# Kernel tuning notes

Hardware: AMD Instinct MI355X
Metric: run time of the kernel (lower is better)

## Reference

```python
import jax, jax.numpy as jnp
import numpy as np

B, S, H, DH = 4, 2048, 16, 64
D = H * DH          # 1024
EXP = 2
FF_IN = EXP * D * 2  # 4096 (SwiGLU doubles)
FF_HID = EXP * D     # 2048
SCALE_BASE = 512
LN_EPS = 1e-5


def setup_inputs() -> dict:
    key = jax.random.key(0)
    ks = jax.random.split(key, 8)
    inp = {
        "q": jax.random.normal(ks[0], (B, S, D), jnp.float32),
        "k": jax.random.normal(ks[1], (B, S, D), jnp.float32),
        "v": jax.random.normal(ks[2], (B, S, D), jnp.float32),
        "Wqkv": jax.random.normal(ks[3], (D, 3 * D), jnp.float32) * (1.0 / np.sqrt(D)),
        "bqkv": jnp.zeros((3 * D,), jnp.float32),
        "q_scale": jnp.ones((DH,), jnp.float32),
        "k_scale": jnp.ones((DH,), jnp.float32),
        "ln_g": jnp.ones((D,), jnp.float32),
        "ln_b": jnp.zeros((D,), jnp.float32),
        "W1": jax.random.normal(ks[4], (D, FF_IN), jnp.float32) * (1.0 / np.sqrt(D)),
        "b1": jnp.zeros((FF_IN,), jnp.float32),
        "W2": jax.random.normal(ks[5], (FF_HID, D), jnp.float32) * (1.0 / np.sqrt(FF_HID)),
        "b2": jnp.zeros((D,), jnp.float32),
    }
    return inp


def rotate_half(x):
    x1, x2 = jnp.split(x, 2, axis=-1)
    return jnp.concatenate((-x2, x1), axis=-1)


def apply_rope(pos, t, scale):
    # pos: [S, DH], scale: [S, DH] (broadcast over [B, H, S, DH])
    return t * jnp.cos(pos) * scale + rotate_half(t) * jnp.sin(pos) * scale


def rotary_tables(seq_len):
    inv_freq = 1.0 / (10000.0 ** (jnp.arange(0, DH, 2, dtype=jnp.float32) / DH))
    t = jnp.arange(seq_len, dtype=jnp.float32)
    freqs = t[:, None] * inv_freq[None, :]            # [S, DH/2]
    freqs = jnp.concatenate((freqs, freqs), axis=-1)  # [S, DH]
    power = (t - seq_len // 2) / SCALE_BASE           # [S]
    base = (jnp.arange(0, DH, 2, dtype=jnp.float32) + 0.4 * DH) / (1.4 * DH)  # [DH/2]
    scale = base[None, :] ** power[:, None]           # [S, DH/2]
    scale = jnp.concatenate((scale, scale), axis=-1)  # [S, DH]
    return freqs, scale


def l2norm(x, eps=1e-12):
    n = jnp.sqrt(jnp.sum(x * x, axis=-1, keepdims=True))
    return x / jnp.maximum(n, eps)


def reference(q, k, v, Wqkv, bqkv, q_scale, k_scale, ln_g, ln_b, W1, b1, W2, b2):
    del k, v  # module projects qkv from q; k,v args are unused (faithful to source)
    n, seq_len, _ = q.shape
    qkv = q @ Wqkv + bqkv                              # [B, S, 3D]
    qkv = qkv.reshape(n, seq_len, H, 3 * DH).transpose(0, 2, 1, 3)  # [B, H, S, 3DH]
    q_, k_, v_ = jnp.split(qkv, 3, axis=-1)
    q_ = l2norm(q_) * q_scale
    k_ = l2norm(k_) * k_scale
    pos, xscale = rotary_tables(seq_len)
    q_ = apply_rope(pos, q_, xscale)
    k_ = apply_rope(pos, k_, 1.0 / xscale)
    # scaled dot product attention (non-causal)
    scores = jnp.einsum("bhid,bhjd->bhij", q_, k_) / np.sqrt(DH)
    attn = jax.nn.softmax(scores, axis=-1)
    out = jnp.einsum("bhij,bhjd->bhid", attn, v_)      # [B, H, S, DH]
    out = out.transpose(0, 2, 1, 3).reshape(n, seq_len, D)
    # LayerNorm
    mu = jnp.mean(out, axis=-1, keepdims=True)
    var = jnp.mean((out - mu) ** 2, axis=-1, keepdims=True)
    out = (out - mu) / jnp.sqrt(var + LN_EPS) * ln_g + ln_b
    # SwiGLU FFN (dropout = identity in eval)
    h = out @ W1 + b1                                  # [B, S, FF_IN]
    x_, gate = jnp.split(h, 2, axis=-1)
    ff = (jax.nn.silu(gate) * x_) @ W2 + b2            # [B, S, D]
    return out + ff
```

## Files before the change

### kernel.cpp

```cpp
#include <hip/hip_runtime.h>
#include <math.h>


typedef __bf16 bf16;
typedef bf16 bf16x8 __attribute__((ext_vector_type(8)));
typedef bf16 bf16x4 __attribute__((ext_vector_type(4)));
typedef float f32x4 __attribute__((ext_vector_type(4)));

#define MFMA(a, b, c) __builtin_amdgcn_mfma_f32_16x16x32_bf16(a, b, c, 0, 0, 0)

__device__ __forceinline__ void async16(const void* g, void* l) {
    __builtin_amdgcn_global_load_lds(
        (const __attribute__((address_space(1))) void*)g,
        (__attribute__((address_space(3))) void*)l,
        16, 0, 0);
}

__global__ __launch_bounds__(256) void fill_sentinel(float* __restrict__ o)
{
    size_t i = ((size_t)blockIdx.x * 256 + threadIdx.x) * 4;
    *(float4*)&o[i] = make_float4(0.25f, 0.25f, 0.25f, 0.25f);
}

__global__ __launch_bounds__(256) void convert_f32_bf16(
    const float* __restrict__ in, bf16* __restrict__ out)
{
    size_t i = ((size_t)blockIdx.x * 256 + threadIdx.x) * 8;
    float4 f0 = *(const float4*)&in[i];
    float4 f1 = *(const float4*)&in[i + 4];
    bf16x8 v;
    v[0] = (bf16)f0.x; v[1] = (bf16)f0.y; v[2] = (bf16)f0.z; v[3] = (bf16)f0.w;
    v[4] = (bf16)f1.x; v[5] = (bf16)f1.y; v[6] = (bf16)f1.z; v[7] = (bf16)f1.w;
    *(bf16x8*)&out[i] = v;
}

__global__ __launch_bounds__(256) void transpose_f32_bf16(
    const float* __restrict__ in, bf16* __restrict__ out, int K, int N)
{
    __shared__ bf16 T[64][70];
    const int tN = N >> 6;
    const int tk = blockIdx.x / tN, tn = blockIdx.x % tN;
    const int k0 = tk << 6, n0 = tn << 6;
    const int t = threadIdx.x;
    const int r = t >> 2, c0 = (t & 3) << 4;
    const float* src = &in[(size_t)(k0 + r) * N + n0 + c0];
    for (int j = 0; j < 4; ++j) {
        float4 f = *(const float4*)(src + 4 * j);
        T[r][c0 + 4 * j + 0] = (bf16)f.x;
        T[r][c0 + 4 * j + 1] = (bf16)f.y;
        T[r][c0 + 4 * j + 2] = (bf16)f.z;
        T[r][c0 + 4 * j + 3] = (bf16)f.w;
    }
    __syncthreads();
    bf16x8 o0, o1;
    for (int i = 0; i < 8; ++i) o0[i] = T[c0 + i][r];
    for (int i = 0; i < 8; ++i) o1[i] = T[c0 + 8 + i][r];
    *(bf16x8*)&out[(size_t)(n0 + r) * K + k0 + c0]     = o0;
    *(bf16x8*)&out[(size_t)(n0 + r) * K + k0 + c0 + 8] = o1;
}

__global__ __launch_bounds__(256) void transpose_v(
    const bf16* __restrict__ in, bf16* __restrict__ out)
{
    __shared__ bf16 T[64][72];
    const int bh = blockIdx.x >> 5;
    const int s0 = (blockIdx.x & 31) << 6;
    const bf16* ip = in + ((size_t)bh << 17) + (size_t)s0 * 64;
    bf16* op = out + ((size_t)bh << 17) + s0;
    const int t = threadIdx.x;
    const int r = t >> 2, c0 = (t & 3) << 4;
    *(bf16x8*)&T[r][c0]     = *(const bf16x8*)&ip[r * 64 + c0];
    *(bf16x8*)&T[r][c0 + 8] = *(const bf16x8*)&ip[r * 64 + c0 + 8];
    __syncthreads();
    bf16x8 o0, o1;
    for (int i = 0; i < 8; ++i) o0[i] = T[c0 + i][r];
    for (int i = 0; i < 8; ++i) o1[i] = T[c0 + 8 + i][r];
    *(bf16x8*)&op[(size_t)r * 2048 + c0]     = o0;
    *(bf16x8*)&op[(size_t)r * 2048 + c0 + 8] = o1;
}

template <int BN, bool SPLIT>
__device__ __forceinline__ void g256_stage(
    const bf16* __restrict__ Ag, const bf16* __restrict__ Bg, int kt,
    int lda, int K, char* aB, char* bB, int tid, int wave)
{
    for (int i = 0; i < 4; ++i) {
        int l = (i << 9) + tid;
        int r = l >> 3;
        int cbs = ((l & 7) ^ (r & 7)) << 3;
        int cu = (i << 9) + (wave << 6);
        async16(&Ag[(size_t)r * lda + kt + cbs], aB + (size_t)cu * 16);
    }
    for (int i = 0; i < BN / 64; ++i) {
        int l = (i << 9) + tid;
        int r = l >> 3;
        int cbs = ((l & 7) ^ (r & 7)) << 3;
        int cu = (i << 9) + (wave << 6);
        size_t grow = SPLIT ? (size_t)(r + ((r >> 7) * 1920)) : (size_t)r;
        async16(&Bg[grow * K + kt + cbs], bB + (size_t)cu * 16);
    }
}

template <int NI, bool SPLIT>
__device__ __forceinline__ void g256_compute(
    const bf16* At, const bf16* Bt, f32x4 (&acc)[8][NI],
    int wm, int wn, int l16, int quad, int rsw)
{
    for (int kd = 0; kd < 2; ++kd) {
        bf16x8 af[8], bfr[NI];
        for (int mi = 0; mi < 8; ++mi) {
            int row = (wm << 7) + (mi << 4) + l16;
            af[mi] = *(const bf16x8*)&At[(row << 6) + ((((kd << 2) + quad) ^ rsw) << 3)];
        }
        for (int ni = 0; ni < NI; ++ni) {
            int row;
            if (SPLIT)
                row = ((ni >= 2) ? 128 : 0) + (wn << 5) + ((ni & 1) << 4) + l16;
            else
                row = wn * (NI << 4) + (ni << 4) + l16;
            bfr[ni] = *(const bf16x8*)&Bt[(row << 6) + ((((kd << 2) + quad) ^ rsw) << 3)];
        }
        __builtin_amdgcn_s_setprio(1);
        for (int mi = 0; mi < 8; ++mi)
            for (int ni = 0; ni < NI; ++ni)
                acc[mi][ni] = MFMA(af[mi], bfr[ni], acc[mi][ni]);
        __builtin_amdgcn_s_setprio(0);
    }
}

#define G256_WAIT()                                                        \
    if constexpr (BN == 256) asm volatile("s_waitcnt vmcnt(8)" ::: "memory"); \
    else                     asm volatile("s_waitcnt vmcnt(6)" ::: "memory")

template <int EPI, int BN>
__global__ __launch_bounds__(512, 2) void gemm256(
    const bf16* __restrict__ A, const bf16* __restrict__ BT,
    const float* __restrict__ bias, int M, int N, int K, int lda,
    bf16* __restrict__ C0, bf16* __restrict__ C1, bf16* __restrict__ C2,
    float* __restrict__ Cf, const bf16* __restrict__ resid)
{
    constexpr int NI = BN / 64;
    constexpr bool SPLIT = (EPI == 3);
    constexpr int TILE_N = SPLIT ? 128 : BN;
    __shared__ bf16 As[2][256 * 64];
    __shared__ bf16 Bs[2][BN * 64];
    const int tid = threadIdx.x;
    const int lane = tid & 63, wave = tid >> 6;
    const int quad = lane >> 4, l16 = lane & 15;
    const int rsw = l16 & 7;
    const int wm = wave >> 2, wn = wave & 3;
    const int nb = N / TILE_N;
    const int nwg = gridDim.x;
    const int bid = blockIdx.x;
    const int swz = (bid & 7) * (nwg >> 3) + (bid >> 3);
    const int bm = swz / nb, bn = swz % nb;
    const int m0 = bm << 8, n0 = bn * TILE_N;
    const bf16* Ag = A + (size_t)m0 * lda;
    const bf16* Bg = BT + (size_t)n0 * K;
    char* a0 = (char*)&As[0][0]; char* a1 = (char*)&As[1][0];
    char* b0 = (char*)&Bs[0][0]; char* b1 = (char*)&Bs[1][0];

    f32x4 acc[8][NI] = {};
    const int NT = K >> 6;

    g256_stage<BN, SPLIT>(Ag, Bg, 0,  lda, K, a0, b0, tid, wave);
    g256_stage<BN, SPLIT>(Ag, Bg, 64, lda, K, a1, b1, tid, wave);
    G256_WAIT();
    __builtin_amdgcn_s_barrier();

    for (int t = 0; t < NT; t += 2) {
        g256_compute<NI, SPLIT>(&As[0][0], &Bs[0][0], acc, wm, wn, l16, quad, rsw);
        asm volatile("" ::: "memory");
        __builtin_amdgcn_s_barrier();
        if (t + 2 < NT) {
            g256_stage<BN, SPLIT>(Ag, Bg, (t + 2) << 6, lda, K, a0, b0, tid, wave);
            G256_WAIT();
        } else {
            asm volatile("s_waitcnt vmcnt(0)" ::: "memory");
        }
        __builtin_amdgcn_s_barrier();
        g256_compute<NI, SPLIT>(&As[1][0], &Bs[1][0], acc, wm, wn, l16, quad, rsw);
        asm volatile("" ::: "memory");
        __builtin_amdgcn_s_barrier();
        if (t + 3 < NT) {
            g256_stage<BN, SPLIT>(Ag, Bg, (t + 3) << 6, lda, K, a1, b1, tid, wave);
            G256_WAIT();
        } else {
            asm volatile("s_waitcnt vmcnt(0)" ::: "memory");
        }
        __builtin_amdgcn_s_barrier();
    }

    if (EPI == 3) {
        for (int mi = 0; mi < 8; ++mi) {
            for (int ni = 0; ni < 2; ++ni) {
                for (int r = 0; r < 4; ++r) {
                    int row  = m0 + (wm << 7) + (mi << 4) + (quad << 2) + r;
                    int colx = n0 + (wn << 5) + (ni << 4) + l16;
                    float x = acc[mi][ni][r]     + bias[colx];
                    float g = acc[mi][ni + 2][r] + bias[2048 + colx];
                    float s = g / (1.0f + __expf(-g)) * x;
                    C0[(size_t)row * N + colx] = (bf16)s;
                }
            }
        }
        return;
    }

    for (int mi = 0; mi < 8; ++mi) {
        for (int ni = 0; ni < NI; ++ni) {
            for (int r = 0; r < 4; ++r) {
                int row = m0 + (wm << 7) + (mi << 4) + (quad << 2) + r;
                int col = n0 + wn * (NI << 4) + (ni << 4) + l16;
                float v = acc[mi][ni][r] + bias[col];
                if (EPI == 0) {
                    int b = row >> 11, s = row & 2047;
                    int h = col / 192, w = col % 192;
                    int tq = w >> 6, d = w & 63;
                    bf16* dst = (tq == 0) ? C0 : (tq == 1) ? C1 : C2;
                    dst[((((size_t)b * 16 + h) * 2048 + s) << 6) + d] = (bf16)v;
                } else if (EPI == 1) {
                    C0[(size_t)row * N + col] = (bf16)v;
                } else {
                    float rv = (float)resid[(size_t)row * N + col];
                    Cf[(size_t)row * N + col] = v + rv;
                }
            }
        }
    }
}

__global__ __launch_bounds__(256) void norm_rope(
    bf16* __restrict__ qb, bf16* __restrict__ kb,
    const float* __restrict__ qs, const float* __restrict__ ks)
{
    const int wave = threadIdx.x >> 6, lane = threadIdx.x & 63;
    const int rid = blockIdx.x * 4 + wave;
    const bool is_k = rid >= 131072;
    const int idx = is_k ? rid - 131072 : rid;
    const int s = idx & 2047;
    bf16* ptr = (is_k ? kb : qb) + ((size_t)idx << 6);
    const int d = lane;

    float v = (float)ptr[d];
    float ss = v * v;
    for (int o = 1; o < 64; o <<= 1) ss += __shfl_xor(ss, o);
    float t = v * rsqrtf(fmaxf(ss, 1e-24f));
    t *= (is_k ? ks : qs)[d];

    float partner = __shfl_xor(t, 32);
    float rh = (d < 32) ? -partner : partner;

    const float fi = (float)(d & 31);
    float inv_freq = __builtin_amdgcn_exp2f(fi * -0.4152410118609203f);
    float pos = (float)s * inv_freq;
    float rev = pos * 0.15915494309189535f;
    rev = rev - floorf(rev);
    float sn = __builtin_amdgcn_sinf(rev);
    float cs = __builtin_amdgcn_cosf(rev);
    float base = (2.0f * fi + 25.6f) * (1.0f / 89.6f);
    float power = ((float)s - 1024.0f) * (1.0f / 512.0f);
    if (is_k) power = -power;
    float xsc = __builtin_amdgcn_exp2f(power * __builtin_amdgcn_logf(base));
    ptr[d] = (bf16)((t * cs + rh * sn) * xsc);
}

__device__ __forceinline__ int swz_a(int r) {
    int a = (r >> 3) & 3;
    return (r & 7) ^ a ^ ((a << 1) & 7);
}

__device__ __forceinline__ void attn_stage(
    const bf16* __restrict__ Kp, const bf16* __restrict__ Vp, int kt,
    char* kB, char* vB, int tid, int wave)
{
    for (int i = 0; i < 2; ++i) {
        int l = (i << 8) + tid;
        int r = l >> 3;
        int cbs = ((l & 7) ^ swz_a(r)) << 3;
        int cu = (i << 8) + (wave << 6);
        async16(&Kp[(size_t)(kt + r) * 64 + cbs], kB + (size_t)cu * 16);
        async16(&Vp[(size_t)r * 2048 + kt + cbs], vB + (size_t)cu * 16);
    }
}

__global__ __launch_bounds__(256) void attn(
    const bf16* __restrict__ Q, const bf16* __restrict__ Kb,
    const bf16* __restrict__ VT, bf16* __restrict__ O)
{
    __shared__ bf16 Ks[2][64 * 64];
    __shared__ bf16 Vt[2][64 * 64];
    const int tid = threadIdx.x;
    const int lane = tid & 63, wave = tid >> 6;
    const int quad = lane >> 4, l16 = lane & 15;
    const int wgi = blockIdx.x;
    const int rr = wgi >> 3;
    const int bh = ((wgi & 7) << 3) + (rr >> 4);
    const int q0 = (rr & 15) << 7;
    const int s_base = q0 + (wave << 5);
    const bf16* Qp = Q + ((size_t)bh << 17);
    const bf16* Kp = Kb + ((size_t)bh << 17);
    const bf16* Vp = VT + ((size_t)bh << 17);

    bf16x8 qf[2][2];
    for (int sub = 0; sub < 2; ++sub) {
        const bf16* qrow = Qp + (size_t)(s_base + (sub << 4) + l16) * 64;
        qf[sub][0] = *(const bf16x8*)&qrow[(quad << 3)];
        qf[sub][1] = *(const bf16x8*)&qrow[32 + (quad << 3)];
        for (int j = 0; j < 8; ++j) {
            qf[sub][0][j] = (bf16)((float)qf[sub][0][j] * 0.1803368801f);
            qf[sub][1][j] = (bf16)((float)qf[sub][1][j] * 0.1803368801f);
        }
    }
    bf16x8 ones = {};
    if (l16 == 0) for (int j = 0; j < 8; ++j) ones[j] = (bf16)1.0f;

    f32x4 oacc[2][4] = {};
    f32x4 lacc[2] = {};

    attn_stage(Kp, Vp, 0, (char*)&Ks[0][0], (char*)&Vt[0][0], tid, wave);

    int buf = 0;
    for (int kt = 0; kt < 2048; kt += 64, buf ^= 1) {
        __syncthreads();
        if (kt + 64 < 2048)
            attn_stage(Kp, Vp, kt + 64,
                       (char*)&Ks[buf ^ 1][0], (char*)&Vt[buf ^ 1][0], tid, wave);

        const bf16* Kt_ = &Ks[buf][0];
        const bf16* Vc_ = &Vt[buf][0];

        bf16x8 pf0[2], pf1[2];
        for (int nt = 0; nt < 4; ++nt) {
            const int g = ((l16 >> 2) << 3) + (l16 & 3)
                        + ((nt & 1) << 2) + ((nt >> 1) << 5);
            const int gs = swz_a(g);
            bf16x8 kf0 = *(const bf16x8*)&Kt_[(g << 6) + ((quad ^ gs) << 3)];
            bf16x8 kf1 = *(const bf16x8*)&Kt_[(g << 6) + (((quad + 4) ^ gs) << 3)];
            __builtin_amdgcn_s_setprio(1);
            for (int sub = 0; sub < 2; ++sub) {
                f32x4 z = {};
                z = MFMA(kf0, qf[sub][0], z);
                z = MFMA(kf1, qf[sub][1], z);
                bf16x8& dst = (nt < 2) ? pf0[sub] : pf1[sub];
                const int jb = (nt & 1) << 2;
                for (int r = 0; r < 4; ++r)
                    dst[jb + r] = (bf16)__builtin_amdgcn_exp2f(z[r]);
            }
            __builtin_amdgcn_s_setprio(0);
        }

        __builtin_amdgcn_s_setprio(1);
        for (int ntd = 0; ntd < 4; ++ntd) {
            int row = (ntd << 4) + l16;
            int vs = swz_a(row);
            bf16x8 vf0 = *(const bf16x8*)&Vc_[(row << 6) + ((quad ^ vs) << 3)];
            bf16x8 vf1 = *(const bf16x8*)&Vc_[(row << 6) + (((quad + 4) ^ vs) << 3)];
            for (int sub = 0; sub < 2; ++sub) {
                oacc[sub][ntd] = MFMA(pf0[sub], vf0, oacc[sub][ntd]);
                oacc[sub][ntd] = MFMA(pf1[sub], vf1, oacc[sub][ntd]);
            }
        }
        for (int sub = 0; sub < 2; ++sub) {
            lacc[sub] = MFMA(pf0[sub], ones, lacc[sub]);
            lacc[sub] = MFMA(pf1[sub], ones, lacc[sub]);
        }
        __builtin_amdgcn_s_setprio(0);
    }

    const int b = bh >> 4, h = bh & 15;
    for (int sub = 0; sub < 2; ++sub)
        for (int r = 0; r < 4; ++r) {
            float l = __shfl(lacc[sub][r], quad << 4);
            float inv_l = 1.0f / l;
            int srow = s_base + (sub << 4) + (quad << 2) + r;
            for (int ntd = 0; ntd < 4; ++ntd) {
                int d = (ntd << 4) + l16;
                O[((((size_t)b * 2048 + srow) * 16) + h) * 64 + d] =
                    (bf16)(oacc[sub][ntd][r] * inv_l);
            }
        }
}

__global__ __launch_bounds__(256) void layernorm(
    const bf16* __restrict__ x, const float* __restrict__ g,
    const float* __restrict__ b, bf16* __restrict__ y)
{
    __shared__ float red[8];
    const int row = blockIdx.x;
    const int t = threadIdx.x;
    const bf16* xr = x + ((size_t)row << 10);
    bf16x4 xv = *(const bf16x4*)&xr[t << 2];
    float v[4], s = 0.0f, sq = 0.0f;
    for (int i = 0; i < 4; ++i) { v[i] = (float)xv[i]; s += v[i]; sq += v[i] * v[i]; }
    for (int o = 1; o < 64; o <<= 1) { s += __shfl_xor(s, o); sq += __shfl_xor(sq, o); }
    const int wave = t >> 6, lane = t & 63;
    if (lane == 0) { red[wave] = s; red[4 + wave] = sq; }
    __syncthreads();
    s  = red[0] + red[1] + red[2] + red[3];
    sq = red[4] + red[5] + red[6] + red[7];
    float mu = s * (1.0f / 1024.0f);
    float var = fmaxf(sq * (1.0f / 1024.0f) - mu * mu, 0.0f);
    float rstd = rsqrtf(var + 1e-5f);
    bf16x4 ov;
    for (int i = 0; i < 4; ++i) {
        int c = (t << 2) + i;
        ov[i] = (bf16)((v[i] - mu) * rstd * g[c] + b[c]);
    }
    *(bf16x4*)(y + ((size_t)row << 10) + (t << 2)) = ov;
}

extern "C" void kernel_launch(void* const* d_in, const int* in_sizes, int n_in,
                              void* d_out, int out_size, void* d_ws, size_t ws_size,
                              hipStream_t stream) {
    (void)in_sizes; (void)n_in; (void)out_size;
    const float* q    = (const float*)d_in[0];
    const float* Wqkv = (const float*)d_in[3];
    const float* bqkv = (const float*)d_in[4];
    const float* qsc  = (const float*)d_in[5];
    const float* ksc  = (const float*)d_in[6];
    const float* lng  = (const float*)d_in[7];
    const float* lnb  = (const float*)d_in[8];
    const float* W1   = (const float*)d_in[9];
    const float* b1   = (const float*)d_in[10];
    const float* W2   = (const float*)d_in[11];
    const float* b2   = (const float*)d_in[12];
    float* out = (float*)d_out;

    const size_t MB = 1024 * 1024;
    if (ws_size < 92 * MB) {
        fill_sentinel<<<8192, 256, 0, stream>>>(out);
        return;
    }

    char* ws = (char*)d_ws;
    bf16* W2T      = (bf16*)(ws + 0);
    bf16* ln_buf   = (bf16*)(ws + 4  * MB);
    bf16* q_bf     = (bf16*)(ws + 4  * MB);
    bf16* W1T      = (bf16*)(ws + 20 * MB);
    bf16* q_buf    = (bf16*)(ws + 28 * MB);
    bf16* k_buf    = (bf16*)(ws + 44 * MB);
    bf16* v_buf    = (bf16*)(ws + 60 * MB);
    bf16* WqkvT    = (bf16*)(ws + 76 * MB);
    bf16* vt_buf   = (bf16*)(ws + 76 * MB);
    bf16* attn_buf = (bf16*)(ws + 60 * MB);
    bf16* h_buf    = (bf16*)(ws + 28 * MB);

    convert_f32_bf16<<<4096, 256, 0, stream>>>(q, q_bf);
    transpose_f32_bf16<<<512,  256, 0, stream>>>(W2,   W2T,   2048, 1024);
    transpose_f32_bf16<<<1024, 256, 0, stream>>>(W1,   W1T,   1024, 4096);
    transpose_f32_bf16<<<768,  256, 0, stream>>>(Wqkv, WqkvT, 1024, 3072);

    gemm256<0, 128><<<768, 512, 0, stream>>>(q_bf, WqkvT, bqkv, 8192, 3072, 1024, 1024,
                                             q_buf, k_buf, v_buf, nullptr, nullptr);
    norm_rope<<<65536, 256, 0, stream>>>(q_buf, k_buf, qsc, ksc);
    transpose_v<<<2048, 256, 0, stream>>>(v_buf, vt_buf);
    attn<<<1024, 256, 0, stream>>>(q_buf, k_buf, vt_buf, attn_buf);
    layernorm<<<8192, 256, 0, stream>>>(attn_buf, lng, lnb, ln_buf);
    gemm256<3, 256><<<512, 512, 0, stream>>>(ln_buf, W1T, b1, 8192, 2048, 1024, 1024,
                                             h_buf, nullptr, nullptr, nullptr, nullptr);
    gemm256<2, 128><<<256, 512, 0, stream>>>(h_buf, W2T, b2, 8192, 1024, 2048, 2048,
                                             nullptr, nullptr, nullptr, out, ln_buf);
}
```

Baseline: 489.5 us.

## Fuse V transpose into QKV GEMM epilogue and halve attention query tile

```diff
diff --git a/kernel.cpp b/kernel.cpp
--- a/kernel.cpp
+++ b/kernel.cpp
@@ -57,26 +57,6 @@
     for (int i = 0; i < 8; ++i) o1[i] = T[c0 + 8 + i][r];
     *(bf16x8*)&out[(size_t)(n0 + r) * K + k0 + c0]     = o0;
     *(bf16x8*)&out[(size_t)(n0 + r) * K + k0 + c0 + 8] = o1;
-}
-
-__global__ __launch_bounds__(256) void transpose_v(
-    const bf16* __restrict__ in, bf16* __restrict__ out)
-{
-    __shared__ bf16 T[64][72];
-    const int bh = blockIdx.x >> 5;
-    const int s0 = (blockIdx.x & 31) << 6;
-    const bf16* ip = in + ((size_t)bh << 17) + (size_t)s0 * 64;
-    bf16* op = out + ((size_t)bh << 17) + s0;
-    const int t = threadIdx.x;
-    const int r = t >> 2, c0 = (t & 3) << 4;
-    *(bf16x8*)&T[r][c0]     = *(const bf16x8*)&ip[r * 64 + c0];
-    *(bf16x8*)&T[r][c0 + 8] = *(const bf16x8*)&ip[r * 64 + c0 + 8];
-    __syncthreads();
-    bf16x8 o0, o1;
-    for (int i = 0; i < 8; ++i) o0[i] = T[c0 + i][r];
-    for (int i = 0; i < 8; ++i) o1[i] = T[c0 + 8 + i][r];
-    *(bf16x8*)&op[(size_t)r * 2048 + c0]     = o0;
-    *(bf16x8*)&op[(size_t)r * 2048 + c0 + 8] = o1;
 }
 
 template <int BN, bool SPLIT>
@@ -207,19 +187,39 @@
         return;
     }
 
+    if (EPI == 0) {
+        for (int mi = 0; mi < 8; ++mi) {
+            for (int ni = 0; ni < NI; ++ni) {
+                int row0 = m0 + (wm << 7) + (mi << 4) + (quad << 2);
+                int col  = n0 + wn * (NI << 4) + (ni << 4) + l16;
+                int b  = row0 >> 11, s0 = row0 & 2047;
+                int h  = col / 192, w = col % 192;
+                int tq = w >> 6, d = w & 63;
+                int bh = b * 16 + h;
+                float bia = bias[col];
+                if (tq == 2) {
+                    bf16x4 pk;
+                    for (int r = 0; r < 4; ++r)
+                        pk[r] = (bf16)(acc[mi][ni][r] + bia);
+                    *(bf16x4*)&C2[((size_t)bh << 17) + (size_t)d * 2048 + s0] = pk;
+                } else {
+                    bf16* dst = (tq == 0) ? C0 : C1;
+                    for (int r = 0; r < 4; ++r)
+                        dst[(((size_t)bh * 2048 + s0 + r) << 6) + d] =
+                            (bf16)(acc[mi][ni][r] + bia);
+                }
+            }
+        }
+        return;
+    }
+
     for (int mi = 0; mi < 8; ++mi) {
         for (int ni = 0; ni < NI; ++ni) {
             for (int r = 0; r < 4; ++r) {
                 int row = m0 + (wm << 7) + (mi << 4) + (quad << 2) + r;
                 int col = n0 + wn * (NI << 4) + (ni << 4) + l16;
                 float v = acc[mi][ni][r] + bias[col];
-                if (EPI == 0) {
-                    int b = row >> 11, s = row & 2047;
-                    int h = col / 192, w = col % 192;
-                    int tq = w >> 6, d = w & 63;
-                    bf16* dst = (tq == 0) ? C0 : (tq == 1) ? C1 : C2;
-                    dst[((((size_t)b * 16 + h) * 2048 + s) << 6) + d] = (bf16)v;
-                } else if (EPI == 1) {
+                if (EPI == 1) {
                     C0[(size_t)row * N + col] = (bf16)v;
                 } else {
                     float rv = (float)resid[(size_t)row * N + col];
@@ -295,28 +295,28 @@
     const int quad = lane >> 4, l16 = lane & 15;
     const int wgi = blockIdx.x;
     const int rr = wgi >> 3;
-    const int bh = ((wgi & 7) << 3) + (rr >> 4);
-    const int q0 = (rr & 15) << 7;
-    const int s_base = q0 + (wave << 5);
+    const int bh = ((wgi & 7) << 3) + (rr >> 5);
+    const int q0 = (rr & 31) << 6;
+    const int s_base = q0 + (wave << 4);
     const bf16* Qp = Q + ((size_t)bh << 17);
     const bf16* Kp = Kb + ((size_t)bh << 17);
     const bf16* Vp = VT + ((size_t)bh << 17);
 
-    bf16x8 qf[2][2];
-    for (int sub = 0; sub < 2; ++sub) {
-        const bf16* qrow = Qp + (size_t)(s_base + (sub << 4) + l16) * 64;
-        qf[sub][0] = *(const bf16x8*)&qrow[(quad << 3)];
-        qf[sub][1] = *(const bf16x8*)&qrow[32 + (quad << 3)];
+    bf16x8 qf[2];
+    {
+        const bf16* qrow = Qp + (size_t)(s_base + l16) * 64;
+        qf[0] = *(const bf16x8*)&qrow[(quad << 3)];
+        qf[1] = *(const bf16x8*)&qrow[32 + (quad << 3)];
         for (int j = 0; j < 8; ++j) {
-            qf[sub][0][j] = (bf16)((float)qf[sub][0][j] * 0.1803368801f);
-            qf[sub][1][j] = (bf16)((float)qf[sub][1][j] * 0.1803368801f);
+            qf[0][j] = (bf16)((float)qf[0][j] * 0.1803368801f);
+            qf[1][j] = (bf16)((float)qf[1][j] * 0.1803368801f);
         }
     }
     bf16x8 ones = {};
     if (l16 == 0) for (int j = 0; j < 8; ++j) ones[j] = (bf16)1.0f;
 
-    f32x4 oacc[2][4] = {};
-    f32x4 lacc[2] = {};
+    f32x4 oacc[4] = {};
+    f32x4 lacc = {};
 
     attn_stage(Kp, Vp, 0, (char*)&Ks[0][0], (char*)&Vt[0][0], tid, wave);
 
@@ -330,7 +330,7 @@
         const bf16* Kt_ = &Ks[buf][0];
         const bf16* Vc_ = &Vt[buf][0];
 
-        bf16x8 pf0[2], pf1[2];
+        bf16x8 pf0, pf1;
         for (int nt = 0; nt < 4; ++nt) {
             const int g = ((l16 >> 2) << 3) + (l16 & 3)
                         + ((nt & 1) << 2) + ((nt >> 1) << 5);
@@ -338,16 +338,14 @@
             bf16x8 kf0 = *(const bf16x8*)&Kt_[(g << 6) + ((quad ^ gs) << 3)];
             bf16x8 kf1 = *(const bf16x8*)&Kt_[(g << 6) + (((quad + 4) ^ gs) << 3)];
             __builtin_amdgcn_s_setprio(1);
-            for (int sub = 0; sub < 2; ++sub) {
-                f32x4 z = {};
-                z = MFMA(kf0, qf[sub][0], z);
-                z = MFMA(kf1, qf[sub][1], z);
-                bf16x8& dst = (nt < 2) ? pf0[sub] : pf1[sub];
-                const int jb = (nt & 1) << 2;
-                for (int r = 0; r < 4; ++r)
-                    dst[jb + r] = (bf16)__builtin_amdgcn_exp2f(z[r]);
-            }
+            f32x4 z = {};
+            z = MFMA(kf0, qf[0], z);
+            z = MFMA(kf1, qf[1], z);
             __builtin_amdgcn_s_setprio(0);
+            bf16x8& dst = (nt < 2) ? pf0 : pf1;
+            const int jb = (nt & 1) << 2;
+            for (int r = 0; r < 4; ++r)
+                dst[jb + r] = (bf16)__builtin_amdgcn_exp2f(z[r]);
         }
 
         __builtin_amdgcn_s_setprio(1);
@@ -356,30 +354,25 @@
             int vs = swz_a(row);
             bf16x8 vf0 = *(const bf16x8*)&Vc_[(row << 6) + ((quad ^ vs) << 3)];
             bf16x8 vf1 = *(const bf16x8*)&Vc_[(row << 6) + (((quad + 4) ^ vs) << 3)];
-            for (int sub = 0; sub < 2; ++sub) {
-                oacc[sub][ntd] = MFMA(pf0[sub], vf0, oacc[sub][ntd]);
-                oacc[sub][ntd] = MFMA(pf1[sub], vf1, oacc[sub][ntd]);
-            }
-        }
-        for (int sub = 0; sub < 2; ++sub) {
-            lacc[sub] = MFMA(pf0[sub], ones, lacc[sub]);
-            lacc[sub] = MFMA(pf1[sub], ones, lacc[sub]);
-        }
+            oacc[ntd] = MFMA(pf0, vf0, oacc[ntd]);
+            oacc[ntd] = MFMA(pf1, vf1, oacc[ntd]);
+        }
+        lacc = MFMA(pf0, ones, lacc);
+        lacc = MFMA(pf1, ones, lacc);
         __builtin_amdgcn_s_setprio(0);
     }
 
     const int b = bh >> 4, h = bh & 15;
-    for (int sub = 0; sub < 2; ++sub)
-        for (int r = 0; r < 4; ++r) {
-            float l = __shfl(lacc[sub][r], quad << 4);
-            float inv_l = 1.0f / l;
-            int srow = s_base + (sub << 4) + (quad << 2) + r;
-            for (int ntd = 0; ntd < 4; ++ntd) {
-                int d = (ntd << 4) + l16;
-                O[((((size_t)b * 2048 + srow) * 16) + h) * 64 + d] =
-                    (bf16)(oacc[sub][ntd][r] * inv_l);
-            }
-        }
+    for (int r = 0; r < 4; ++r) {
+        float l = __shfl(lacc[r], quad << 4);
+        float inv_l = 1.0f / l;
+        int srow = s_base + (quad << 2) + r;
+        for (int ntd = 0; ntd < 4; ++ntd) {
+            int d = (ntd << 4) + l16;
+            O[((((size_t)b * 2048 + srow) * 16) + h) * 64 + d] =
+                (bf16)(oacc[ntd][r] * inv_l);
+        }
+    }
 }
 
 __global__ __launch_bounds__(256) void layernorm(
@@ -440,10 +433,9 @@
     bf16* W1T      = (bf16*)(ws + 20 * MB);
     bf16* q_buf    = (bf16*)(ws + 28 * MB);
     bf16* k_buf    = (bf16*)(ws + 44 * MB);
-    bf16* v_buf    = (bf16*)(ws + 60 * MB);
+    bf16* vt_buf   = (bf16*)(ws + 60 * MB);
     bf16* WqkvT    = (bf16*)(ws + 76 * MB);
-    bf16* vt_buf   = (bf16*)(ws + 76 * MB);
-    bf16* attn_buf = (bf16*)(ws + 60 * MB);
+    bf16* attn_buf = (bf16*)(ws + 76 * MB);
     bf16* h_buf    = (bf16*)(ws + 28 * MB);
 
     convert_f32_bf16<<<4096, 256, 0, stream>>>(q, q_bf);
@@ -452,10 +444,9 @@
     transpose_f32_bf16<<<768,  256, 0, stream>>>(Wqkv, WqkvT, 1024, 3072);
 
     gemm256<0, 128><<<768, 512, 0, stream>>>(q_bf, WqkvT, bqkv, 8192, 3072, 1024, 1024,
-                                             q_buf, k_buf, v_buf, nullptr, nullptr);
+                                             q_buf, k_buf, vt_buf, nullptr, nullptr);
     norm_rope<<<65536, 256, 0, stream>>>(q_buf, k_buf, qsc, ksc);
-    transpose_v<<<2048, 256, 0, stream>>>(v_buf, vt_buf);
-    attn<<<1024, 256, 0, stream>>>(q_buf, k_buf, vt_buf, attn_buf);
+    attn<<<2048, 256, 0, stream>>>(q_buf, k_buf, vt_buf, attn_buf);
     layernorm<<<8192, 256, 0, stream>>>(attn_buf, lng, lnb, ln_buf);
     gemm256<3, 256><<<512, 512, 0, stream>>>(ln_buf, W1T, b1, 8192, 2048, 1024, 1024,
                                              h_buf, nullptr, nullptr, nullptr, nullptr);
```

New measurement: 486.0 us. No clear change (-0.7%).
